# Kernel tuning notes

Measured on AMD Instinct MI355X. Metric: run time of the kernel, lower is better.

## Reference

```python
import jax, jax.numpy as jnp
import numpy as np

C = 256      # in_channel
H = 8        # attention heads
B = 256      # number of graphs in the batch
S = 256      # max nodes per graph (dense batch length)
N = B * S - 100   # total nodes (last graph partially filled -> real padding mask)
E = 1_000_000     # total edges
EPS = 1e-5        # BatchNorm eps


def setup_inputs() -> dict:
    key = jax.random.key(0)
    ks = jax.random.split(key, 24)
    nrm = lambda k, shape: jax.random.normal(k, shape, jnp.float32) * 0.02
    x = jax.random.normal(ks[0], (N, C), jnp.float32)
    edge_index = jax.random.randint(ks[1], (2, E), 0, N)
    batch = jnp.minimum(jnp.arange(N) // S, B - 1)  # sorted graph ids, sizes <= S
    inp = {
        'x': x, 'edge_index': edge_index, 'batch': batch,
        # local GraphConv (PyG-style): W_root x_i + W_nei sum_j x_j + b_nei
        'W_root': nrm(ks[2], (C, C)), 'W_nei': nrm(ks[3], (C, C)), 'b_nei': jnp.zeros((C,), jnp.float32),
        # MultiheadAttention packed in/out projections
        'Wqkv': nrm(ks[4], (3 * C, C)), 'bqkv': jnp.zeros((3 * C,), jnp.float32),
        'Wo': nrm(ks[5], (C, C)), 'bo': jnp.zeros((C,), jnp.float32),
        # MLP: Linear(C,2C) -> ReLU -> Linear(2C,C)
        'W1': nrm(ks[6], (2 * C, C)), 'b1': jnp.zeros((2 * C,), jnp.float32),
        'W2': nrm(ks[7], (C, 2 * C)), 'b2': jnp.zeros((C,), jnp.float32),
    }
    # three BatchNorm1d layers (inference mode: running stats)
    for i, (kg, kv) in enumerate(((ks[8], ks[9]), (ks[10], ks[11]), (ks[12], ks[13])), start=1):
        inp[f'g{i}'] = 1.0 + nrm(kg, (C,))
        inp[f'be{i}'] = jnp.zeros((C,), jnp.float32)
        inp[f'm{i}'] = nrm(kv, (C,))
        inp[f'v{i}'] = jax.random.uniform(jax.random.fold_in(kv, 1), (C,), jnp.float32, 0.5, 1.5)
    return inp


def reference(x, edge_index, batch, W_root, W_nei, b_nei, Wqkv, bqkv, Wo, bo,
              W1, b1, W2, b2, g1, be1, m1, v1, g2, be2, m2, v2, g3, be3, m3, v3):
    def bn(h, g, b, m, v):
        return (h - m) * (g * jax.lax.rsqrt(v + EPS)) + b

    # --- local message passing conv + residual + BN (dropout = identity, eval) ---
    src, dst = edge_index[0], edge_index[1]
    agg = jax.ops.segment_sum(x[src], dst, num_segments=N)        # [N, C]
    h = agg @ W_nei.T + b_nei + x @ W_root.T
    h1 = bn(h + x, g1, be1, m1, v1)

    # --- to_dense_batch(x, batch) ---
    counts = jax.ops.segment_sum(jnp.ones((N,), jnp.int32), batch, num_segments=B)
    starts = jnp.concatenate([jnp.zeros((1,), jnp.int32), jnp.cumsum(counts)[:-1].astype(jnp.int32)])
    pos = jnp.arange(N) - starts[batch]                            # position within graph
    dense = jnp.zeros((B, S, C), x.dtype).at[batch, pos].set(x)    # [B, S, C]
    mask = jnp.zeros((B, S), bool).at[batch, pos].set(True)

    # --- MultiheadAttention(dense, dense, dense, key_padding_mask=~mask) ---
    qkv = dense @ Wqkv.T + bqkv
    q, k, v = jnp.split(qkv, 3, axis=-1)
    Dh = C // H
    q = q.reshape(B, S, H, Dh)
    k = k.reshape(B, S, H, Dh)
    v = v.reshape(B, S, H, Dh)
    scores = jnp.einsum('bqhd,bkhd->bhqk', q, k) / jnp.sqrt(jnp.float32(Dh))
    scores = jnp.where(mask[:, None, None, :], scores, jnp.float32(-1e9))
    probs = jax.nn.softmax(scores, axis=-1)
    attn = jnp.einsum('bhqk,bkhd->bqhd', probs, v).reshape(B, S, C)
    attn = attn @ Wo.T + bo

    # gather back h[mask] (row-major order == node order since batch is sorted)
    h2 = bn(attn[batch, pos] + x, g2, be2, m2, v2)

    # --- sum of branches + residual MLP + BN ---
    out = h1 + h2
    mlp = jax.nn.relu(out @ W1.T + b1) @ W2.T + b2
    return bn(out + mlp, g3, be3, m3, v3)
```

## Files before the change

kernel.cpp:

```cpp
#include <hip/hip_runtime.h>
#include <hip/hip_bf16.h>

typedef __attribute__((ext_vector_type(8))) short bf16x8;
typedef __attribute__((ext_vector_type(4))) float f32x4;
typedef unsigned short u16;
typedef unsigned int u32;

#define BN_EPS 1e-5f
#define NBINS 65536

__device__ __forceinline__ float b2f(u16 u) {
    u32 x = ((u32)u) << 16;
    float f; __builtin_memcpy(&f, &x, 4); return f;
}
__device__ __forceinline__ u16 f2b(float f) {
    f = fminf(fmaxf(f, -3.0e38f), 3.0e38f);
    __hip_bfloat16 h = __float2bfloat16(f);
    u16 s; __builtin_memcpy(&s, &h, 2); return s;
}
__device__ __forceinline__ bf16x8 cvt8(f32x4 a, f32x4 b) {
    bf16x8 r;
    r[0] = (short)f2b(a[0]); r[1] = (short)f2b(a[1]);
    r[2] = (short)f2b(a[2]); r[3] = (short)f2b(a[3]);
    r[4] = (short)f2b(b[0]); r[5] = (short)f2b(b[1]);
    r[6] = (short)f2b(b[2]); r[7] = (short)f2b(b[3]);
    return r;
}
#define MFMA(a, b, c) __builtin_amdgcn_mfma_f32_16x16x32_bf16((a), (b), (c), 0, 0, 0)

__global__ __launch_bounds__(256) void k_cvtw(const float* __restrict__ src,
                                              u16* __restrict__ dst, int n) {
    const int i = blockIdx.x * 256 + threadIdx.x;
    if (i < n) dst[i] = f2b(src[i]);
}
__global__ __launch_bounds__(256) void k_cvtx(const float* __restrict__ src,
                                              u16* __restrict__ dst, int n4) {
    const int i = blockIdx.x * 256 + threadIdx.x;
    if (i < n4) {
        const f32x4 v = ((const f32x4*)src)[i];
        ushort4 pk;
        pk.x = f2b(v[0]); pk.y = f2b(v[1]); pk.z = f2b(v[2]); pk.w = f2b(v[3]);
        ((ushort4*)dst)[i] = pk;
    }
}

__global__ __launch_bounds__(256) void k_hist(
    const int* __restrict__ edst, int* __restrict__ counts, int E) {
    const int i = blockIdx.x * 256 + threadIdx.x;
    if (i < E) atomicAdd(&counts[edst[i]], 1);
}

__global__ __launch_bounds__(1024) void k_scan(
    const int* __restrict__ counts, int* __restrict__ start,
    int* __restrict__ cursor) {
    __shared__ int sums[1024];
    const int t = threadIdx.x;
    const int base = t * 64;
    int s = 0;
#pragma unroll 8
    for (int j = 0; j < 64; ++j) s += counts[base + j];
    sums[t] = s;
    __syncthreads();
    for (int off = 1; off < 1024; off <<= 1) {
        const int tmp = (t >= off) ? sums[t - off] : 0;
        __syncthreads();
        sums[t] += tmp;
        __syncthreads();
    }
    int run = sums[t] - s;
    for (int j = 0; j < 64; ++j) {
        start[base + j] = run;
        cursor[base + j] = run;
        run += counts[base + j];
    }
    if (t == 1023) start[NBINS] = run;
}

__global__ __launch_bounds__(256) void k_reorder(
    const int* __restrict__ esrc, const int* __restrict__ edst,
    int* __restrict__ cursor, int* __restrict__ ssrc, int E) {
    const int i = blockIdx.x * 256 + threadIdx.x;
    if (i < E) {
        const int p = atomicAdd(&cursor[edst[i]], 1);
        ssrc[p] = esrc[i];
    }
}

__global__ __launch_bounds__(256) void k_aggregate(
    const u16* __restrict__ xb, const int* __restrict__ ssrc,
    const int* __restrict__ start, u16* __restrict__ agg,
    int lo, int hi) {
    const int rel = (blockIdx.x << 2) + (threadIdx.x >> 6);
    const int r = lo + rel;
    if (r >= hi) return;
    const int lane = threadIdx.x & 63;
    const int s0 = start[r], s1 = start[r + 1];
    f32x4 acc = {0.f, 0.f, 0.f, 0.f};
    int j = s0;
    int sNext = (j < s1) ? ssrc[j] : 0;
    while (j < s1) {
        const int s = sNext;
        ++j;
        if (j < s1) sNext = ssrc[j];
        const ushort4 xv = *(const ushort4*)(xb + (size_t)s * 256 + lane * 4);
        acc[0] += b2f(xv.x); acc[1] += b2f(xv.y);
        acc[2] += b2f(xv.z); acc[3] += b2f(xv.w);
    }
    ushort4 pk;
    pk.x = f2b(acc[0]); pk.y = f2b(acc[1]); pk.z = f2b(acc[2]); pk.w = f2b(acc[3]);
    *(ushort4*)(agg + (size_t)rel * 256 + lane * 4) = pk;
}

template<bool ABF16>
__device__ __forceinline__ void gemm_acc(const void* A, int lda, int Mload,
                                         const u16* W, int K,
                                         int rowBase, int colBase,
                                         f32x4 (&acc)[2][4])
{
    const int lane = threadIdx.x & 63;
    const int r16 = lane & 15;
    const int quad = lane >> 4;
    int r0 = rowBase + r16;
    int r1 = rowBase + 16 + r16;
    const bool z0 = (r0 >= Mload), z1 = (r1 >= Mload);
    if (z0) r0 = 0;
    if (z1) r1 = 0;
    const bf16x8 zf = {0,0,0,0,0,0,0,0};
    for (int kk = 0; kk < K; kk += 32) {
        const int ko = kk + quad * 8;
        bf16x8 a0, a1;
        if (ABF16) {
            const u16* Ab = (const u16*)A;
            a0 = *(const bf16x8*)(Ab + (size_t)r0 * lda + ko);
            a1 = *(const bf16x8*)(Ab + (size_t)r1 * lda + ko);
        } else {
            const float* Af = (const float*)A;
            const f32x4* p0 = (const f32x4*)(Af + (size_t)r0 * lda + ko);
            const f32x4* p1 = (const f32x4*)(Af + (size_t)r1 * lda + ko);
            a0 = cvt8(p0[0], p0[1]);
            a1 = cvt8(p1[0], p1[1]);
        }
        if (z0) a0 = zf;
        if (z1) a1 = zf;
#pragma unroll
        for (int nt = 0; nt < 4; ++nt) {
            const bf16x8 b = *(const bf16x8*)(W + (size_t)(colBase + nt * 16 + r16) * K + ko);
            acc[0][nt] = MFMA(a0, b, acc[0][nt]);
            acc[1][nt] = MFMA(a1, b, acc[1][nt]);
        }
    }
}

__global__ __launch_bounds__(256) void k_attn(
    const u16* __restrict__ xb, const u16* __restrict__ Wqkv,
    const float* __restrict__ bqkv, u16* __restrict__ attnOut,
    int lo, int N, int ngraph)
{
    __shared__ u16 ks_s[256 * 40];
    __shared__ u16 vt_s[32 * 264];
    __shared__ u16 sc_s[4 * 1280];
    int brel, h;
    if ((ngraph & 7) == 0) {
        const int x8 = blockIdx.x & 7;
        const int j  = blockIdx.x >> 3;
        h = j & 7;
        brel = x8 + 8 * (j >> 3);
    } else {
        brel = blockIdx.x >> 3;
        h = blockIdx.x & 7;
    }
    const int base = lo + brel * 256;
    const int count = min(256, N - base);
    const int t = threadIdx.x;
    const int wave = t >> 6;
    const int lane = t & 63;
    const int r16 = lane & 15;
    const int quad = lane >> 4;
    u16* msc = sc_s + wave * 1280;
    u16* qsc = ks_s + wave * 64 * 40;
    const float scale = 0.17677669529663687f;

    bf16x8 qa[4];

#pragma unroll
    for (int sel = 0; sel < 3; ++sel) {
        f32x4 acc[4][2] = {};
        for (int kk = 0; kk < 256; kk += 32) {
            const int ko = kk + quad * 8;
            bf16x8 a[4];
#pragma unroll
            for (int mt = 0; mt < 4; ++mt) {
                int row = base + wave * 64 + mt * 16 + r16;
                row = min(row, N - 1);
                a[mt] = *(const bf16x8*)(xb + (size_t)row * 256 + ko);
            }
#pragma unroll
            for (int nt = 0; nt < 2; ++nt) {
                const int wrow = sel * 256 + h * 32 + nt * 16 + r16;
                const bf16x8 b = *(const bf16x8*)(Wqkv + (size_t)wrow * 256 + ko);
#pragma unroll
                for (int mt = 0; mt < 4; ++mt)
                    acc[mt][nt] = MFMA(a[mt], b, acc[mt][nt]);
            }
        }
        if (sel == 0) {
#pragma unroll
            for (int nt = 0; nt < 2; ++nt) {
                const float bias = bqkv[h * 32 + nt * 16 + r16];
#pragma unroll
                for (int mt = 0; mt < 4; ++mt)
#pragma unroll
                    for (int r = 0; r < 4; ++r)
                        qsc[(mt * 16 + quad * 4 + r) * 40 + nt * 16 + r16] =
                            f2b((acc[mt][nt][r] + bias) * scale);
            }
#pragma unroll
            for (int mt = 0; mt < 4; ++mt)
                qa[mt] = *(const bf16x8*)(qsc + (mt * 16 + r16) * 40 + quad * 8);
        } else if (sel == 1) {
#pragma unroll
            for (int nt = 0; nt < 2; ++nt) {
                const float bias = bqkv[256 + h * 32 + nt * 16 + r16];
#pragma unroll
                for (int mt = 0; mt < 4; ++mt)
#pragma unroll
                    for (int r = 0; r < 4; ++r) {
                        const int key = wave * 64 + mt * 16 + quad * 4 + r;
                        ks_s[key * 40 + nt * 16 + r16] = f2b(acc[mt][nt][r] + bias);
                    }
            }
        } else {
#pragma unroll
            for (int nt = 0; nt < 2; ++nt) {
                const int d = nt * 16 + r16;
                const float bias = bqkv[512 + h * 32 + d];
#pragma unroll
                for (int mt = 0; mt < 4; ++mt) {
                    const int key0 = wave * 64 + mt * 16 + quad * 4;
                    ushort4 pk;
                    pk.x = f2b(acc[mt][nt][0] + bias);
                    pk.y = f2b(acc[mt][nt][1] + bias);
                    pk.z = f2b(acc[mt][nt][2] + bias);
                    pk.w = f2b(acc[mt][nt][3] + bias);
                    *(ushort4*)(vt_s + d * 264 + key0) = pk;
                }
            }
        }
    }
    __syncthreads();

#pragma unroll
    for (int mp = 0; mp < 2; ++mp) {
        f32x4 O[2][2] = {};
        f32x4 rs[2] = {};
        for (int kb = 0; kb < 8; ++kb) {
            bf16x8 bk[2];
#pragma unroll
            for (int nt = 0; nt < 2; ++nt)
                bk[nt] = *(const bf16x8*)(ks_s + (kb * 32 + nt * 16 + r16) * 40 + quad * 8);
            f32x4 S[2][2] = {};
#pragma unroll
            for (int mt = 0; mt < 2; ++mt)
#pragma unroll
                for (int nt = 0; nt < 2; ++nt)
                    S[mt][nt] = MFMA(qa[mp * 2 + mt], bk[nt], S[mt][nt]);
#pragma unroll
            for (int mt = 0; mt < 2; ++mt)
#pragma unroll
                for (int nt = 0; nt < 2; ++nt) {
                    const int key = kb * 32 + nt * 16 + r16;
                    const bool kv = (key < count);
#pragma unroll
                    for (int r = 0; r < 4; ++r) {
                        const float s = fminf(fmaxf(S[mt][nt][r], -60.f), 60.f);
                        const float e = kv ? __expf(s) : 0.f;
                        rs[mt][r] += e;
                        msc[(mt * 16 + quad * 4 + r) * 40 + nt * 16 + r16] = f2b(e);
                    }
                }
            bf16x8 ap[2], bv[2];
#pragma unroll
            for (int mt = 0; mt < 2; ++mt)
                ap[mt] = *(const bf16x8*)(msc + (mt * 16 + r16) * 40 + quad * 8);
#pragma unroll
            for (int nt = 0; nt < 2; ++nt)
                bv[nt] = *(const bf16x8*)(vt_s + (nt * 16 + r16) * 264 + kb * 32 + quad * 8);
#pragma unroll
            for (int mt = 0; mt < 2; ++mt)
#pragma unroll
                for (int nt = 0; nt < 2; ++nt)
                    O[mt][nt] = MFMA(ap[mt], bv[nt], O[mt][nt]);
        }
#pragma unroll
        for (int mt = 0; mt < 2; ++mt)
#pragma unroll
            for (int r = 0; r < 4; ++r) {
                float v = rs[mt][r];
                v += __shfl_xor(v, 1, 16);
                v += __shfl_xor(v, 2, 16);
                v += __shfl_xor(v, 4, 16);
                v += __shfl_xor(v, 8, 16);
                rs[mt][r] = v;
            }
#pragma unroll
        for (int mt = 0; mt < 2; ++mt) {
#pragma unroll
            for (int nt = 0; nt < 2; ++nt)
#pragma unroll
                for (int r = 0; r < 4; ++r) {
                    const float inv = 1.f / fmaxf(rs[mt][r], 1e-30f);
                    const int qrow = wave * 64 + mp * 32 + mt * 16 + quad * 4 + r;
                    attnOut[(size_t)(brel * 256 + qrow) * 256 + h * 32 + nt * 16 + r16]
                        = f2b(O[mt][nt][r] * inv);
                }
        }
    }
}

__global__ __launch_bounds__(256) void k_out2(
    const u16* __restrict__ attn, const u16* __restrict__ Wo,
    const float* __restrict__ bo, const float* __restrict__ x,
    const float* __restrict__ g2, const float* __restrict__ be2,
    const float* __restrict__ m2, const float* __restrict__ v2,
    float* __restrict__ dout, int lo, int hi)
{
    const int wave = threadIdx.x >> 6;
    const int rowBase = blockIdx.y * 128 + wave * 32;
    const int colBase = blockIdx.x * 64;
    const int ML = hi - lo;
    f32x4 acc[2][4] = {};
    gemm_acc<true>(attn, 256, ML, Wo, 256, rowBase, colBase, acc);
    const int lane = threadIdx.x & 63;
    const int r16 = lane & 15, quad = lane >> 4;
#pragma unroll
    for (int nt = 0; nt < 4; ++nt) {
        const int col = colBase + nt * 16 + r16;
        const float bias = bo[col];
        const float mm = m2[col];
        const float sc = g2[col] * rsqrtf(v2[col] + BN_EPS);
        const float bb = be2[col];
#pragma unroll
        for (int tt = 0; tt < 2; ++tt) {
#pragma unroll
            for (int r = 0; r < 4; ++r) {
                const int rel = rowBase + tt * 16 + quad * 4 + r;
                if (rel < ML) {
                    const size_t idx = (size_t)(lo + rel) * 256 + col;
                    const float val = acc[tt][nt][r] + bias + x[idx];
                    dout[idx] = (val - mm) * sc + bb;
                }
            }
        }
    }
}

__global__ __launch_bounds__(256) void k_conv(
    const u16* __restrict__ agg, const u16* __restrict__ xb,
    const float* __restrict__ x,
    const u16* __restrict__ Wnei, const u16* __restrict__ Wroot,
    const float* __restrict__ bnei,
    const float* __restrict__ g1, const float* __restrict__ be1,
    const float* __restrict__ m1, const float* __restrict__ v1,
    float* __restrict__ dout, int lo, int hi)
{
    const int wave = threadIdx.x >> 6;
    const int rowBase = blockIdx.y * 128 + wave * 32;
    const int colBase = blockIdx.x * 64;
    const int ML = hi - lo;
    f32x4 acc[2][4] = {};
    gemm_acc<true>(agg, 256, ML, Wnei, 256, rowBase, colBase, acc);
    gemm_acc<true>(xb + (size_t)lo * 256, 256, ML, Wroot, 256, rowBase, colBase, acc);
    const int lane = threadIdx.x & 63;
    const int r16 = lane & 15, quad = lane >> 4;
#pragma unroll
    for (int nt = 0; nt < 4; ++nt) {
        const int col = colBase + nt * 16 + r16;
        const float bias = bnei[col];
        const float mm = m1[col];
        const float sc = g1[col] * rsqrtf(v1[col] + BN_EPS);
        const float bb = be1[col];
#pragma unroll
        for (int tt = 0; tt < 2; ++tt) {
#pragma unroll
            for (int r = 0; r < 4; ++r) {
                const int rel = rowBase + tt * 16 + quad * 4 + r;
                if (rel < ML) {
                    const size_t idx = (size_t)(lo + rel) * 256 + col;
                    const float val = acc[tt][nt][r] + bias + x[idx];
                    dout[idx] += (val - mm) * sc + bb;
                }
            }
        }
    }
}

__global__ __launch_bounds__(256) void k_mlp(
    const u16* __restrict__ W1, const float* __restrict__ b1,
    const u16* __restrict__ W2, const float* __restrict__ b2v,
    const float* __restrict__ g3, const float* __restrict__ be3,
    const float* __restrict__ m3, const float* __restrict__ v3,
    float* __restrict__ dout, int N)
{
    __shared__ u16 as[64 * 264];
    __shared__ u16 ts[64 * 136];
    const int rowBase = blockIdx.x * 64;
    const int t = threadIdx.x;
    const int wave = t >> 6;
    const int lane = t & 63;
    const int r16 = lane & 15;
    const int quad = lane >> 4;

#pragma unroll
    for (int i = t; i < 64 * 64; i += 256) {
        const int row = i >> 6;
        const int c4 = i & 63;
        int grow = rowBase + row;
        grow = min(grow, N - 1);
        const f32x4 v = *(const f32x4*)(dout + (size_t)grow * 256 + c4 * 4);
        ushort4 pk;
        pk.x = f2b(v[0]); pk.y = f2b(v[1]); pk.z = f2b(v[2]); pk.w = f2b(v[3]);
        *(ushort4*)(as + row * 264 + c4 * 4) = pk;
    }
    __syncthreads();

    f32x4 yacc[4][4] = {};

    for (int s = 0; s < 4; ++s) {
        f32x4 a1[4][2] = {};
        for (int kk = 0; kk < 256; kk += 32) {
            const int ko = kk + quad * 8;
            bf16x8 a[4];
#pragma unroll
            for (int mt = 0; mt < 4; ++mt)
                a[mt] = *(const bf16x8*)(as + (mt * 16 + r16) * 264 + ko);
#pragma unroll
            for (int nt = 0; nt < 2; ++nt) {
                const int wrow = s * 128 + wave * 32 + nt * 16 + r16;
                const bf16x8 b = *(const bf16x8*)(W1 + (size_t)wrow * 256 + ko);
#pragma unroll
                for (int mt = 0; mt < 4; ++mt)
                    a1[mt][nt] = MFMA(a[mt], b, a1[mt][nt]);
            }
        }
        __syncthreads();
#pragma unroll
        for (int nt = 0; nt < 2; ++nt) {
            const int col = wave * 32 + nt * 16 + r16;
            const float bias = b1[s * 128 + col];
#pragma unroll
            for (int mt = 0; mt < 4; ++mt) {
#pragma unroll
                for (int r = 0; r < 4; ++r) {
                    const int row = mt * 16 + quad * 4 + r;
                    ts[row * 136 + col] = f2b(fmaxf(a1[mt][nt][r] + bias, 0.f));
                }
            }
        }
        __syncthreads();
        for (int kk = 0; kk < 128; kk += 32) {
            const int ko = kk + quad * 8;
            bf16x8 a[4];
#pragma unroll
            for (int mt = 0; mt < 4; ++mt)
                a[mt] = *(const bf16x8*)(ts + (mt * 16 + r16) * 136 + ko);
#pragma unroll
            for (int nt = 0; nt < 4; ++nt) {
                const int wrow = wave * 64 + nt * 16 + r16;
                const bf16x8 b = *(const bf16x8*)(W2 + (size_t)wrow * 512 + s * 128 + ko);
#pragma unroll
                for (int mt = 0; mt < 4; ++mt)
                    yacc[mt][nt] = MFMA(a[mt], b, yacc[mt][nt]);
            }
        }
    }
#pragma unroll
    for (int nt = 0; nt < 4; ++nt) {
        const int col = wave * 64 + nt * 16 + r16;
        const float bias = b2v[col];
        const float mm = m3[col];
        const float sc = g3[col] * rsqrtf(v3[col] + BN_EPS);
        const float bb = be3[col];
#pragma unroll
        for (int mt = 0; mt < 4; ++mt) {
#pragma unroll
            for (int r = 0; r < 4; ++r) {
                const int grow = rowBase + mt * 16 + quad * 4 + r;
                if (grow < N) {
                    const size_t idx = (size_t)grow * 256 + col;
                    const float val = yacc[mt][nt][r] + bias + dout[idx];
                    dout[idx] = (val - mm) * sc + bb;
                }
            }
        }
    }
}

extern "C" void kernel_launch(void* const* d_in, const int* in_sizes, int n_in,
                              void* d_out, int out_size, void* d_ws, size_t ws_size,
                              hipStream_t stream)
{
    (void)n_in; (void)out_size;
    const int N = in_sizes[0] / 256;
    const int E = in_sizes[1] / 2;

    const float* x     = (const float*)d_in[0];
    const int*   ei    = (const int*)d_in[1];
    const float* Wroot = (const float*)d_in[3];
    const float* Wnei  = (const float*)d_in[4];
    const float* bnei  = (const float*)d_in[5];
    const float* Wqkv  = (const float*)d_in[6];
    const float* bqkv  = (const float*)d_in[7];
    const float* Wo    = (const float*)d_in[8];
    const float* bo    = (const float*)d_in[9];
    const float* W1    = (const float*)d_in[10];
    const float* b1    = (const float*)d_in[11];
    const float* W2    = (const float*)d_in[12];
    const float* b2    = (const float*)d_in[13];
    const float* g1 = (const float*)d_in[14], *be1 = (const float*)d_in[15];
    const float* m1 = (const float*)d_in[16], *v1  = (const float*)d_in[17];
    const float* g2 = (const float*)d_in[18], *be2 = (const float*)d_in[19];
    const float* m2 = (const float*)d_in[20], *v2  = (const float*)d_in[21];
    const float* g3 = (const float*)d_in[22], *be3 = (const float*)d_in[23];
    const float* m3 = (const float*)d_in[24], *v3  = (const float*)d_in[25];
    float* dout = (float*)d_out;

    u16* wb = (u16*)d_ws;
    u16* Wroot_b = wb;
    u16* Wnei_b  = wb + 65536;
    u16* Wqkv_b  = wb + 131072;
    u16* Wo_b    = wb + 327680;
    u16* W1_b    = wb + 393216;
    u16* W2_b    = wb + 524288;
    const size_t WB_BYTES   = 2u << 20;
    const size_t META_BYTES = 1u << 20;
    const size_t SORT_BYTES = 4u << 20;
    const size_t XB_BYTES   = 32u << 20;
    const size_t FIXED = WB_BYTES + META_BYTES + SORT_BYTES + XB_BYTES;

    int* meta   = (int*)((char*)d_ws + WB_BYTES);
    int* counts = meta;
    int* start  = meta + NBINS;
    int* cursor = start + NBINS + 1;
    int* ssrc   = (int*)((char*)d_ws + WB_BYTES + META_BYTES);
    u16* xb     = (u16*)((char*)d_ws + WB_BYTES + META_BYTES + SORT_BYTES);

    k_cvtw<<<dim3(256),  256, 0, stream>>>(Wroot, Wroot_b, 65536);
    k_cvtw<<<dim3(256),  256, 0, stream>>>(Wnei,  Wnei_b,  65536);
    k_cvtw<<<dim3(768),  256, 0, stream>>>(Wqkv,  Wqkv_b,  196608);
    k_cvtw<<<dim3(256),  256, 0, stream>>>(Wo,    Wo_b,    65536);
    k_cvtw<<<dim3(512),  256, 0, stream>>>(W1,    W1_b,    131072);
    k_cvtw<<<dim3(512),  256, 0, stream>>>(W2,    W2_b,    131072);
    const int n4 = (N * 256) / 4;
    k_cvtx<<<dim3((n4 + 255) / 256), 256, 0, stream>>>(x, xb, n4);

    size_t arena = (ws_size > FIXED) ? (ws_size - FIXED) : 0;
    size_t maxRows = arena / 512;
    int chunkRows = (int)((maxRows < 65536 ? maxRows : 65536) & ~(size_t)255);
    if (chunkRows < 256) chunkRows = 256;

    u16* agg  = (u16*)((char*)d_ws + FIXED);
    u16* attn = agg;

    hipMemsetAsync(counts, 0, NBINS * 4, stream);
    k_hist   <<<dim3((E + 255) / 256), 256, 0, stream>>>(ei + E, counts, E);
    k_scan   <<<dim3(1), 1024, 0, stream>>>(counts, start, cursor);
    k_reorder<<<dim3((E + 255) / 256), 256, 0, stream>>>(ei, ei + E, cursor, ssrc, E);

    for (int lo = 0; lo < N; lo += chunkRows) {
        const int hi = min(lo + chunkRows, N);
        const int ngraph = (hi - lo + 255) / 256;
        k_attn<<<dim3(ngraph * 8), 256, 0, stream>>>(xb, Wqkv_b, bqkv, attn, lo, N, ngraph);
        k_out2<<<dim3(4, (hi - lo + 127) / 128), 256, 0, stream>>>(
            attn, Wo_b, bo, x, g2, be2, m2, v2, dout, lo, hi);
    }
    for (int lo = 0; lo < N; lo += chunkRows) {
        const int hi = min(lo + chunkRows, N);
        k_aggregate<<<dim3((hi - lo + 3) / 4), 256, 0, stream>>>(xb, ssrc, start, agg, lo, hi);
        k_conv<<<dim3(4, (hi - lo + 127) / 128), 256, 0, stream>>>(
            agg, xb, x, Wnei_b, Wroot_b, bnei, g1, be1, m1, v1, dout, lo, hi);
    }
    k_mlp<<<dim3((N + 63) / 64), 256, 0, stream>>>(
        W1_b, b1, W2_b, b2, g3, be3, m3, v3, dout, N);
}
```

Baseline: 861.4 us.

## Keep softmax probabilities in registers and fuse conv and attention output epilogues

The attention inner loop now computes S transposed (keys × queries), so the exp'd probabilities come out in registers already laid out as the A operand of a 16x16x16 MFMA for the PV product. This removes the LDS round-trip through the per-wave score scratch buffer and changes the row-sum reduction to cross-quad shuffles. Separately, the attention output projection and the GraphConv GEMMs are merged into one k_hout kernel that writes h1+h2 once. That drops the read-modify-write of dout and one kernel launch per chunk. In exchange the workspace chunk holds both agg and attn, which halves the chunk size, and it uses the smaller K=16 MFMA for PV.

Result: faster. 820.2 us (-4.8%).

```diff
diff --git a/kernel.cpp b/kernel.cpp
--- a/kernel.cpp
+++ b/kernel.cpp
@@ -2,6 +2,7 @@
 #include <hip/hip_bf16.h>
 
 typedef __attribute__((ext_vector_type(8))) short bf16x8;
+typedef __attribute__((ext_vector_type(4))) short bf16x4;
 typedef __attribute__((ext_vector_type(4))) float f32x4;
 typedef unsigned short u16;
 typedef unsigned int u32;
@@ -27,6 +28,18 @@
     return r;
 }
 #define MFMA(a, b, c) __builtin_amdgcn_mfma_f32_16x16x32_bf16((a), (b), (c), 0, 0, 0)
+
+#if __has_builtin(__builtin_amdgcn_mfma_f32_16x16x16bf16_1k)
+__device__ __forceinline__ f32x4 mfma16(bf16x4 a, bf16x4 b, f32x4 c) {
+    return __builtin_amdgcn_mfma_f32_16x16x16bf16_1k(a, b, c, 0, 0, 0);
+}
+#else
+__device__ __forceinline__ f32x4 mfma16(bf16x4 a, bf16x4 b, f32x4 c) {
+    asm volatile("v_mfma_f32_16x16x16_bf16 %0, %1, %2, %0"
+                 : "+v"(c) : "v"(a), "v"(b));
+    return c;
+}
+#endif
 
 __global__ __launch_bounds__(256) void k_cvtw(const float* __restrict__ src,
                                               u16* __restrict__ dst, int n) {
@@ -158,7 +171,6 @@
 {
     __shared__ u16 ks_s[256 * 40];
     __shared__ u16 vt_s[32 * 264];
-    __shared__ u16 sc_s[4 * 1280];
     int brel, h;
     if ((ngraph & 7) == 0) {
         const int x8 = blockIdx.x & 7;
@@ -176,7 +188,6 @@
     const int lane = t & 63;
     const int r16 = lane & 15;
     const int quad = lane >> 4;
-    u16* msc = sc_s + wave * 1280;
     u16* qsc = ks_s + wave * 64 * 40;
     const float scale = 0.17677669529663687f;
 
@@ -252,74 +263,83 @@
 #pragma unroll
     for (int mp = 0; mp < 2; ++mp) {
         f32x4 O[2][2] = {};
-        f32x4 rs[2] = {};
+        float rs2[2] = {0.f, 0.f};
         for (int kb = 0; kb < 8; ++kb) {
             bf16x8 bk[2];
 #pragma unroll
-            for (int nt = 0; nt < 2; ++nt)
-                bk[nt] = *(const bf16x8*)(ks_s + (kb * 32 + nt * 16 + r16) * 40 + quad * 8);
-            f32x4 S[2][2] = {};
-#pragma unroll
-            for (int mt = 0; mt < 2; ++mt)
-#pragma unroll
-                for (int nt = 0; nt < 2; ++nt)
-                    S[mt][nt] = MFMA(qa[mp * 2 + mt], bk[nt], S[mt][nt]);
-#pragma unroll
-            for (int mt = 0; mt < 2; ++mt)
-#pragma unroll
-                for (int nt = 0; nt < 2; ++nt) {
-                    const int key = kb * 32 + nt * 16 + r16;
-                    const bool kv = (key < count);
+            for (int kt = 0; kt < 2; ++kt)
+                bk[kt] = *(const bf16x8*)(ks_s + (kb * 32 + kt * 16 + r16) * 40 + quad * 8);
+            f32x4 st[2][2];
+#pragma unroll
+            for (int kt = 0; kt < 2; ++kt)
+#pragma unroll
+                for (int mt = 0; mt < 2; ++mt) {
+                    const f32x4 z = {0.f, 0.f, 0.f, 0.f};
+                    st[kt][mt] = MFMA(bk[kt], qa[mp * 2 + mt], z);
+                }
+            bf16x4 pf[2][2];
+#pragma unroll
+            for (int kt = 0; kt < 2; ++kt) {
+                const int key0 = kb * 32 + kt * 16 + quad * 4;
+#pragma unroll
+                for (int mt = 0; mt < 2; ++mt) {
+                    bf16x4 p;
 #pragma unroll
                     for (int r = 0; r < 4; ++r) {
-                        const float s = fminf(fmaxf(S[mt][nt][r], -60.f), 60.f);
-                        const float e = kv ? __expf(s) : 0.f;
-                        rs[mt][r] += e;
-                        msc[(mt * 16 + quad * 4 + r) * 40 + nt * 16 + r16] = f2b(e);
+                        const float s = fminf(fmaxf(st[kt][mt][r], -60.f), 60.f);
+                        const float e = (key0 + r < count) ? __expf(s) : 0.f;
+                        rs2[mt] += e;
+                        p[r] = (short)f2b(e);
                     }
+                    pf[kt][mt] = p;
                 }
-            bf16x8 ap[2], bv[2];
-#pragma unroll
-            for (int mt = 0; mt < 2; ++mt)
-                ap[mt] = *(const bf16x8*)(msc + (mt * 16 + r16) * 40 + quad * 8);
-#pragma unroll
-            for (int nt = 0; nt < 2; ++nt)
-                bv[nt] = *(const bf16x8*)(vt_s + (nt * 16 + r16) * 264 + kb * 32 + quad * 8);
-#pragma unroll
-            for (int mt = 0; mt < 2; ++mt)
-#pragma unroll
-                for (int nt = 0; nt < 2; ++nt)
-                    O[mt][nt] = MFMA(ap[mt], bv[nt], O[mt][nt]);
-        }
-#pragma unroll
-        for (int mt = 0; mt < 2; ++mt)
+            }
+            bf16x4 bv[2][2];
+#pragma unroll
+            for (int kt = 0; kt < 2; ++kt)
+#pragma unroll
+                for (int ntd = 0; ntd < 2; ++ntd)
+                    bv[kt][ntd] = *(const bf16x4*)(vt_s + (ntd * 16 + r16) * 264
+                                                   + kb * 32 + kt * 16 + quad * 4);
+#pragma unroll
+            for (int kt = 0; kt < 2; ++kt)
+#pragma unroll
+                for (int mt = 0; mt < 2; ++mt)
+#pragma unroll
+                    for (int ntd = 0; ntd < 2; ++ntd)
+                        O[mt][ntd] = mfma16(pf[kt][mt], bv[kt][ntd], O[mt][ntd]);
+        }
+#pragma unroll
+        for (int mt = 0; mt < 2; ++mt) {
+            float v = rs2[mt];
+            v += __shfl_xor(v, 16, 64);
+            v += __shfl_xor(v, 32, 64);
+            rs2[mt] = v;
+        }
+#pragma unroll
+        for (int mt = 0; mt < 2; ++mt) {
 #pragma unroll
             for (int r = 0; r < 4; ++r) {
-                float v = rs[mt][r];
-                v += __shfl_xor(v, 1, 16);
-                v += __shfl_xor(v, 2, 16);
-                v += __shfl_xor(v, 4, 16);
-                v += __shfl_xor(v, 8, 16);
-                rs[mt][r] = v;
-            }
-#pragma unroll
-        for (int mt = 0; mt < 2; ++mt) {
-#pragma unroll
-            for (int nt = 0; nt < 2; ++nt)
-#pragma unroll
-                for (int r = 0; r < 4; ++r) {
-                    const float inv = 1.f / fmaxf(rs[mt][r], 1e-30f);
-                    const int qrow = wave * 64 + mp * 32 + mt * 16 + quad * 4 + r;
-                    attnOut[(size_t)(brel * 256 + qrow) * 256 + h * 32 + nt * 16 + r16]
-                        = f2b(O[mt][nt][r] * inv);
-                }
-        }
-    }
-}
-
-__global__ __launch_bounds__(256) void k_out2(
-    const u16* __restrict__ attn, const u16* __restrict__ Wo,
-    const float* __restrict__ bo, const float* __restrict__ x,
+                const float rsv = __shfl(rs2[mt], quad * 4 + r, 16);
+                const float inv = 1.f / fmaxf(rsv, 1e-30f);
+                const int qrow = wave * 64 + mp * 32 + mt * 16 + quad * 4 + r;
+#pragma unroll
+                for (int ntd = 0; ntd < 2; ++ntd)
+                    attnOut[(size_t)(brel * 256 + qrow) * 256 + h * 32 + ntd * 16 + r16]
+                        = f2b(O[mt][ntd][r] * inv);
+            }
+        }
+    }
+}
+
+__global__ __launch_bounds__(256) void k_hout(
+    const u16* __restrict__ attn, const u16* __restrict__ agg,
+    const u16* __restrict__ xbc, const float* __restrict__ x,
+    const u16* __restrict__ Wo, const float* __restrict__ bo,
+    const u16* __restrict__ Wnei, const u16* __restrict__ Wroot,
+    const float* __restrict__ bnei,
+    const float* __restrict__ g1, const float* __restrict__ be1,
+    const float* __restrict__ m1, const float* __restrict__ v1,
     const float* __restrict__ g2, const float* __restrict__ be2,
     const float* __restrict__ m2, const float* __restrict__ v2,
     float* __restrict__ dout, int lo, int hi)
@@ -328,17 +348,24 @@
     const int rowBase = blockIdx.y * 128 + wave * 32;
     const int colBase = blockIdx.x * 64;
     const int ML = hi - lo;
-    f32x4 acc[2][4] = {};
-    gemm_acc<true>(attn, 256, ML, Wo, 256, rowBase, colBase, acc);
+    f32x4 accC[2][4] = {};
+    f32x4 accA[2][4] = {};
+    gemm_acc<true>(agg, 256, ML, Wnei, 256, rowBase, colBase, accC);
+    gemm_acc<true>(xbc, 256, ML, Wroot, 256, rowBase, colBase, accC);
+    gemm_acc<true>(attn, 256, ML, Wo, 256, rowBase, colBase, accA);
     const int lane = threadIdx.x & 63;
     const int r16 = lane & 15, quad = lane >> 4;
 #pragma unroll
     for (int nt = 0; nt < 4; ++nt) {
         const int col = colBase + nt * 16 + r16;
-        const float bias = bo[col];
-        const float mm = m2[col];
-        const float sc = g2[col] * rsqrtf(v2[col] + BN_EPS);
-        const float bb = be2[col];
+        const float b1v = bnei[col];
+        const float mm1 = m1[col];
+        const float sc1 = g1[col] * rsqrtf(v1[col] + BN_EPS);
+        const float bb1 = be1[col];
+        const float b2v = bo[col];
+        const float mm2 = m2[col];
+        const float sc2 = g2[col] * rsqrtf(v2[col] + BN_EPS);
+        const float bb2 = be2[col];
 #pragma unroll
         for (int tt = 0; tt < 2; ++tt) {
 #pragma unroll
@@ -346,48 +373,10 @@
                 const int rel = rowBase + tt * 16 + quad * 4 + r;
                 if (rel < ML) {
                     const size_t idx = (size_t)(lo + rel) * 256 + col;
-                    const float val = acc[tt][nt][r] + bias + x[idx];
-                    dout[idx] = (val - mm) * sc + bb;
-                }
-            }
-        }
-    }
-}
-
-__global__ __launch_bounds__(256) void k_conv(
-    const u16* __restrict__ agg, const u16* __restrict__ xb,
-    const float* __restrict__ x,
-    const u16* __restrict__ Wnei, const u16* __restrict__ Wroot,
-    const float* __restrict__ bnei,
-    const float* __restrict__ g1, const float* __restrict__ be1,
-    const float* __restrict__ m1, const float* __restrict__ v1,
-    float* __restrict__ dout, int lo, int hi)
-{
-    const int wave = threadIdx.x >> 6;
-    const int rowBase = blockIdx.y * 128 + wave * 32;
-    const int colBase = blockIdx.x * 64;
-    const int ML = hi - lo;
-    f32x4 acc[2][4] = {};
-    gemm_acc<true>(agg, 256, ML, Wnei, 256, rowBase, colBase, acc);
-    gemm_acc<true>(xb + (size_t)lo * 256, 256, ML, Wroot, 256, rowBase, colBase, acc);
-    const int lane = threadIdx.x & 63;
-    const int r16 = lane & 15, quad = lane >> 4;
-#pragma unroll
-    for (int nt = 0; nt < 4; ++nt) {
-        const int col = colBase + nt * 16 + r16;
-        const float bias = bnei[col];
-        const float mm = m1[col];
-        const float sc = g1[col] * rsqrtf(v1[col] + BN_EPS);
-        const float bb = be1[col];
-#pragma unroll
-        for (int tt = 0; tt < 2; ++tt) {
-#pragma unroll
-            for (int r = 0; r < 4; ++r) {
-                const int rel = rowBase + tt * 16 + quad * 4 + r;
-                if (rel < ML) {
-                    const size_t idx = (size_t)(lo + rel) * 256 + col;
-                    const float val = acc[tt][nt][r] + bias + x[idx];
-                    dout[idx] += (val - mm) * sc + bb;
+                    const float xv = x[idx];
+                    const float h1 = (accC[tt][nt][r] + b1v + xv - mm1) * sc1 + bb1;
+                    const float h2 = (accA[tt][nt][r] + b2v + xv - mm2) * sc2 + bb2;
+                    dout[idx] = h1 + h2;
                 }
             }
         }
@@ -554,12 +543,12 @@
     k_cvtx<<<dim3((n4 + 255) / 256), 256, 0, stream>>>(x, xb, n4);
 
     size_t arena = (ws_size > FIXED) ? (ws_size - FIXED) : 0;
-    size_t maxRows = arena / 512;
+    size_t maxRows = arena / 1024;
     int chunkRows = (int)((maxRows < 65536 ? maxRows : 65536) & ~(size_t)255);
     if (chunkRows < 256) chunkRows = 256;
 
     u16* agg  = (u16*)((char*)d_ws + FIXED);
-    u16* attn = agg;
+    u16* attn = agg + (size_t)chunkRows * 256;
 
     hipMemsetAsync(counts, 0, NBINS * 4, stream);
     k_hist   <<<dim3((E + 255) / 256), 256, 0, stream>>>(ei + E, counts, E);
@@ -569,15 +558,12 @@
     for (int lo = 0; lo < N; lo += chunkRows) {
         const int hi = min(lo + chunkRows, N);
         const int ngraph = (hi - lo + 255) / 256;
+        k_aggregate<<<dim3((hi - lo + 3) / 4), 256, 0, stream>>>(xb, ssrc, start, agg, lo, hi);
         k_attn<<<dim3(ngraph * 8), 256, 0, stream>>>(xb, Wqkv_b, bqkv, attn, lo, N, ngraph);
-        k_out2<<<dim3(4, (hi - lo + 127) / 128), 256, 0, stream>>>(
-            attn, Wo_b, bo, x, g2, be2, m2, v2, dout, lo, hi);
-    }
-    for (int lo = 0; lo < N; lo += chunkRows) {
-        const int hi = min(lo + chunkRows, N);
-        k_aggregate<<<dim3((hi - lo + 3) / 4), 256, 0, stream>>>(xb, ssrc, start, agg, lo, hi);
-        k_conv<<<dim3(4, (hi - lo + 127) / 128), 256, 0, stream>>>(
-            agg, xb, x, Wnei_b, Wroot_b, bnei, g1, be1, m1, v1, dout, lo, hi);
+        k_hout<<<dim3(4, (hi - lo + 127) / 128), 256, 0, stream>>>(
+            attn, agg, xb + (size_t)lo * 256, x,
+            Wo_b, bo, Wnei_b, Wroot_b, bnei,
+            g1, be1, m1, v1, g2, be2, m2, v2, dout, lo, hi);
     }
     k_mlp<<<dim3((N + 63) / 64), 256, 0, stream>>>(
         W1_b, b1, W2_b, b2, g3, be3, m3, v3, dout, N);
```
